# Optimization experiments

Measured on AMD Instinct MI355X. Metric: run time of the kernel, lower is better.

Reference implementation:

```python
import jax, jax.numpy as jnp
import numpy as np

D_MODEL = 1024
NUM_HEADS = 16
SEQ = 2048
BATCH = 4
THETA = 10000.0
D_K = D_MODEL // NUM_HEADS


def setup_inputs() -> dict:
    key = jax.random.key(0)
    k1, k2, k3, k4, k5 = jax.random.split(key, 5)
    std = np.sqrt(2.0 / (D_MODEL + D_MODEL))
    x = jax.random.normal(k1, (BATCH, SEQ, D_MODEL), dtype=jnp.float32)
    wq = jax.random.normal(k2, (D_MODEL, D_MODEL), dtype=jnp.float32) * std
    wk = jax.random.normal(k3, (D_MODEL, D_MODEL), dtype=jnp.float32) * std
    wv = jax.random.normal(k4, (D_MODEL, D_MODEL), dtype=jnp.float32) * std
    wo = jax.random.normal(k5, (D_MODEL, D_MODEL), dtype=jnp.float32) * std
    token_positions = jnp.arange(SEQ, dtype=jnp.int32)
    return {"x": x, "wq": wq, "wk": wk, "wv": wv, "wo": wo,
            "token_positions": token_positions}


def _apply_rope(t, cos, sin):
    # t: (b, h, s, d_k); cos/sin: (s, d_k/2) -> broadcast over (b, h)
    pairs = t.reshape(*t.shape[:-1], D_K // 2, 2)
    x0, x1 = pairs[..., 0], pairs[..., 1]
    r0 = x0 * cos - x1 * sin
    r1 = x0 * sin + x1 * cos
    return jnp.stack((r0, r1), axis=-1).reshape(t.shape)


def reference(x, wq, wk, wv, wo, token_positions):
    b, s, d = x.shape
    h, dk = NUM_HEADS, D_K

    def split_heads(y):  # (b, s, d) -> (b, h, s, d_k)
        return y.reshape(b, s, h, dk).transpose(0, 2, 1, 3)

    q = split_heads(x @ wq.T)
    k = split_heads(x @ wk.T)
    v = split_heads(x @ wv.T)

    # RoPE tables: angles_j = theta^{-(2j)/d_k}, j = 0..d_k/2-1
    inv_freq = 1.0 / (THETA ** (jnp.arange(0, dk, 2, dtype=jnp.float32) / dk))
    ang = token_positions.astype(jnp.float32)[:, None] * inv_freq[None, :]  # (s, d_k/2)
    cos, sin = jnp.cos(ang), jnp.sin(ang)
    q = _apply_rope(q, cos, sin)
    k = _apply_rope(k, cos, sin)

    scores = jnp.einsum('bhqd,bhkd->bhqk', q, k) / jnp.sqrt(jnp.float32(dk))
    causal = jnp.tril(jnp.ones((s, s), dtype=bool))
    scores = jnp.where(causal, scores, -jnp.inf)
    attn = jax.nn.softmax(scores, axis=-1)
    out = jnp.einsum('bhqk,bhkd->bhqd', attn, v)  # (b, h, s, d_k)
    out = out.transpose(0, 2, 1, 3).reshape(b, s, d)
    return out @ wo.T
```

## Files before the change

### kernel.cpp

```cpp
#include <hip/hip_runtime.h>
#include <stdint.h>

#define B_   4
#define S_   2048
#define H_   16
#define DK_  64
#define DM_  1024
#define M_   (B_ * S_)

typedef __attribute__((ext_vector_type(4)))  float f32x4;
typedef __attribute__((ext_vector_type(16))) float f32x16;
typedef __attribute__((ext_vector_type(8)))  short s16x8;

#define SCQ 0.18033688011112042f

__device__ __forceinline__ uint16_t f2bf(float f) {
    union { float f; uint32_t u; } v; v.f = f;
    uint32_t u = v.u;
    uint32_t r = (u + 0x7FFFu + ((u >> 16) & 1u)) >> 16;
    return (uint16_t)r;
}
__device__ __forceinline__ float bf2f(uint16_t h) {
    union { uint32_t u; float f; } v; v.u = ((uint32_t)h) << 16;
    return v.f;
}
__device__ __forceinline__ uint32_t cvt_pk_bf16(float lo, float hi) {
    uint32_t r;
    asm("v_cvt_pk_bf16_f32 %0, %1, %2" : "=v"(r) : "v"(lo), "v"(hi));
    return r;
}

__device__ __forceinline__ void gload_lds16(const uint16_t* g, uint16_t* l) {
    __builtin_amdgcn_global_load_lds(
        (const __attribute__((address_space(1))) void*)g,
        (__attribute__((address_space(3))) void*)l, 16, 0, 0);
}

__global__ __launch_bounds__(256) void cvt_all(const float* __restrict__ x,
                                               const float* __restrict__ w0,
                                               const float* __restrict__ w1,
                                               const float* __restrict__ w2,
                                               const float* __restrict__ w3,
                                               uint16_t* __restrict__ xo,
                                               uint16_t* __restrict__ o0,
                                               uint16_t* __restrict__ o1,
                                               uint16_t* __restrict__ o2,
                                               uint16_t* __restrict__ o3) {
    const size_t NX = (size_t)M_ * DM_;
    const size_t NW = (size_t)DM_ * DM_;
    size_t i = ((size_t)blockIdx.x * 256 + threadIdx.x) * 4;
    const float* in; uint16_t* out; size_t off;
    if (i < NX) { in = x; out = xo; off = i; }
    else {
        size_t j = i - NX;
        int sel = (int)(j >> 20);
        off = j & (NW - 1);
        in  = sel == 0 ? w0 : sel == 1 ? w1 : sel == 2 ? w2 : w3;
        out = sel == 0 ? o0 : sel == 1 ? o1 : sel == 2 ? o2 : o3;
    }
    float4 v = *reinterpret_cast<const float4*>(in + off);
    ushort4 o;
    o.x = f2bf(v.x); o.y = f2bf(v.y); o.z = f2bf(v.z); o.w = f2bf(v.w);
    *reinterpret_cast<ushort4*>(out + off) = o;
}

__global__ __launch_bounds__(256, 4) void gemm_qkv(const uint16_t* __restrict__ xb,
                                                   const uint16_t* __restrict__ wq,
                                                   const uint16_t* __restrict__ wk,
                                                   const uint16_t* __restrict__ wv,
                                                   uint16_t* __restrict__ qout,
                                                   uint16_t* __restrict__ kout,
                                                   uint16_t* __restrict__ vout) {
    __shared__ uint16_t Al[2][128 * 32];
    __shared__ uint16_t Bl[2][128 * 32];
    const int K = DM_;
    const int lane = threadIdx.x & 63;
    const int w    = threadIdx.x >> 6;
    const int wr   = w >> 1, wc = w & 1;
    const int sel  = blockIdx.x >> 3;
    const int np   = blockIdx.x & 7;
    const int y    = blockIdx.y;
    const int ql   = lane & 31;
    const int hi   = lane >> 5;

    const uint16_t* Aptr; const uint16_t* Bptr;
    int m0, n0;
    if (sel == 2) { Aptr = wv; Bptr = xb; m0 = np * 128; n0 = y * 128; }
    else          { Aptr = xb; Bptr = sel ? wk : wq; m0 = y * 128; n0 = np * 128; }

    const int srow = w * 32 + (lane >> 2);
    const int scol = (((lane & 3) ^ ((lane >> 3) & 3))) * 8;
    const uint16_t* Ag = Aptr + (size_t)(m0 + srow) * K + scol;
    const uint16_t* Bg = Bptr + (size_t)(n0 + srow) * K + scol;
    const int loff = w * 32 * 32;
    const int qsw  = (ql >> 1) & 3;

    f32x16 acc[2][2] = {};
#pragma unroll
    for (int i = 0; i < 2; ++i) {
        gload_lds16(Ag + (size_t)i * 16 * K, &Al[0][loff + i * 16 * 32]);
        gload_lds16(Bg + (size_t)i * 16 * K, &Bl[0][loff + i * 16 * 32]);
    }

    int cur = 0;
    for (int k0 = 0; k0 < K; k0 += 32) {
        __syncthreads();
        if (k0 + 32 < K) {
            const int nb = cur ^ 1, k2 = k0 + 32;
#pragma unroll
            for (int i = 0; i < 2; ++i) {
                gload_lds16(Ag + (size_t)i * 16 * K + k2, &Al[nb][loff + i * 16 * 32]);
                gload_lds16(Bg + (size_t)i * 16 * K + k2, &Bl[nb][loff + i * 16 * 32]);
            }
        }
        s16x8 af[2][2], bfr[2][2];
#pragma unroll
        for (int am = 0; am < 2; ++am)
#pragma unroll
            for (int ks = 0; ks < 2; ++ks)
                af[am][ks] = *reinterpret_cast<const s16x8*>(
                    &Al[cur][(wr * 64 + am * 32 + ql) * 32 + (((ks * 2 + hi) ^ qsw) * 8)]);
#pragma unroll
        for (int bn = 0; bn < 2; ++bn)
#pragma unroll
            for (int ks = 0; ks < 2; ++ks)
                bfr[bn][ks] = *reinterpret_cast<const s16x8*>(
                    &Bl[cur][(wc * 64 + bn * 32 + ql) * 32 + (((ks * 2 + hi) ^ qsw) * 8)]);
#pragma unroll
        for (int am = 0; am < 2; ++am)
#pragma unroll
            for (int bn = 0; bn < 2; ++bn) {
                acc[am][bn] = __builtin_amdgcn_mfma_f32_32x32x16_bf16(af[am][0], bfr[bn][0],
                                                                      acc[am][bn], 0, 0, 0);
                acc[am][bn] = __builtin_amdgcn_mfma_f32_32x32x16_bf16(af[am][1], bfr[bn][1],
                                                                      acc[am][bn], 0, 0, 0);
            }
        cur ^= 1;
    }

#pragma unroll
    for (int am = 0; am < 2; ++am)
#pragma unroll
        for (int bn = 0; bn < 2; ++bn)
#pragma unroll
            for (int r = 0; r < 16; ++r) {
                const int cr = (r & 3) + 8 * (r >> 2);
                int row = m0 + wr * 64 + am * 32 + 4 * hi + cr;
                int col = n0 + wc * 64 + bn * 32 + ql;
                float v = acc[am][bn][r];
                if (sel == 2) {
                    int h = row >> 6,  dk = row & 63;
                    int b = col >> 11, s = col & (S_ - 1);
                    vout[(((size_t)(b * H_ + h)) * DK_ + dk) * S_ + s] = f2bf(v);
                } else {
                    int b = row >> 11, s = row & (S_ - 1);
                    int h = col >> 6,  dk = col & 63;
                    uint16_t bv = f2bf(sel ? v : v * SCQ);
                    (sel ? kout : qout)[(((size_t)(b * H_ + h)) * S_ + s) * DK_ + dk] = bv;
                }
            }
}

__global__ __launch_bounds__(256, 4) void gemm_out(const uint16_t* __restrict__ A,
                                                   const uint16_t* __restrict__ Bm,
                                                   float* __restrict__ Cout,
                                                   int M, int N, int K) {
    __shared__ uint16_t Al[2][128 * 32];
    __shared__ uint16_t Bl[2][128 * 32];
    const int lane = threadIdx.x & 63;
    const int w    = threadIdx.x >> 6;
    const int wr   = w >> 1, wc = w & 1;
    const int m0   = blockIdx.x * 128;
    const int n0   = blockIdx.y * 128;
    const int ql   = lane & 31;
    const int hi   = lane >> 5;

    const int srow = w * 32 + (lane >> 2);
    const int scol = (((lane & 3) ^ ((lane >> 3) & 3))) * 8;
    const uint16_t* Ag = A  + (size_t)(m0 + srow) * K + scol;
    const uint16_t* Bg = Bm + (size_t)(n0 + srow) * K + scol;
    const int loff = w * 32 * 32;
    const int qsw  = (ql >> 1) & 3;

    f32x16 acc[2][2] = {};
#pragma unroll
    for (int i = 0; i < 2; ++i) {
        gload_lds16(Ag + (size_t)i * 16 * K, &Al[0][loff + i * 16 * 32]);
        gload_lds16(Bg + (size_t)i * 16 * K, &Bl[0][loff + i * 16 * 32]);
    }

    int cur = 0;
    for (int k0 = 0; k0 < K; k0 += 32) {
        __syncthreads();
        if (k0 + 32 < K) {
            const int nb = cur ^ 1, k2 = k0 + 32;
#pragma unroll
            for (int i = 0; i < 2; ++i) {
                gload_lds16(Ag + (size_t)i * 16 * K + k2, &Al[nb][loff + i * 16 * 32]);
                gload_lds16(Bg + (size_t)i * 16 * K + k2, &Bl[nb][loff + i * 16 * 32]);
            }
        }
        s16x8 af[2][2], bfr[2][2];
#pragma unroll
        for (int am = 0; am < 2; ++am)
#pragma unroll
            for (int ks = 0; ks < 2; ++ks)
                af[am][ks] = *reinterpret_cast<const s16x8*>(
                    &Al[cur][(wr * 64 + am * 32 + ql) * 32 + (((ks * 2 + hi) ^ qsw) * 8)]);
#pragma unroll
        for (int bn = 0; bn < 2; ++bn)
#pragma unroll
            for (int ks = 0; ks < 2; ++ks)
                bfr[bn][ks] = *reinterpret_cast<const s16x8*>(
                    &Bl[cur][(wc * 64 + bn * 32 + ql) * 32 + (((ks * 2 + hi) ^ qsw) * 8)]);
#pragma unroll
        for (int am = 0; am < 2; ++am)
#pragma unroll
            for (int bn = 0; bn < 2; ++bn) {
                acc[am][bn] = __builtin_amdgcn_mfma_f32_32x32x16_bf16(af[am][0], bfr[bn][0],
                                                                      acc[am][bn], 0, 0, 0);
                acc[am][bn] = __builtin_amdgcn_mfma_f32_32x32x16_bf16(af[am][1], bfr[bn][1],
                                                                      acc[am][bn], 0, 0, 0);
            }
        cur ^= 1;
    }

#pragma unroll
    for (int am = 0; am < 2; ++am)
#pragma unroll
        for (int bn = 0; bn < 2; ++bn)
#pragma unroll
            for (int r = 0; r < 16; ++r) {
                const int cr = (r & 3) + 8 * (r >> 2);
                int row = m0 + wr * 64 + am * 32 + 4 * hi + cr;
                int col = n0 + wc * 64 + bn * 32 + ql;
                Cout[(size_t)row * N + col] = acc[am][bn][r];
            }
}

__global__ __launch_bounds__(256) void rope_kernel(uint16_t* __restrict__ a,
                                                   const int* __restrict__ pos,
                                                   int npairs) {
    int t = blockIdx.x * 256 + threadIdx.x;
    if (t >= npairs) return;
    int j = t & 31;
    int s = (t >> 5) & (S_ - 1);
    float p   = (float)pos[s];
    float inv = exp2f(-(float)j * (13.287712379549449f / 32.0f));
    float ang = p * inv;
    float sn = __sinf(ang);
    float c  = __cosf(ang);
    uint32_t pr = *reinterpret_cast<uint32_t*>(a + (size_t)2 * t);
    float x0 = bf2f((uint16_t)(pr & 0xFFFF));
    float x1 = bf2f((uint16_t)(pr >> 16));
    float r0 = x0 * c - x1 * sn;
    float r1 = x0 * sn + x1 * c;
    uint32_t ot = (uint32_t)f2bf(r0) | ((uint32_t)f2bf(r1) << 16);
    *reinterpret_cast<uint32_t*>(a + (size_t)2 * t) = ot;
}

__global__ __launch_bounds__(256, 2) void flash_attn(const uint16_t* __restrict__ qg,
                                                     const uint16_t* __restrict__ kg,
                                                     const uint16_t* __restrict__ vtg,
                                                     const int* __restrict__ tpos,
                                                     uint16_t* __restrict__ attn) {
    __shared__ __align__(16) uint16_t Kl[2][4096];
    __shared__ __align__(16) uint16_t Vl[2][4096];
    const int lane = threadIdx.x & 63;
    const int w    = threadIdx.x >> 6;
    const int ql   = lane & 31;
    const int hi   = lane >> 5;
    const int id   = blockIdx.x;
    const int bh   = (id & 7) * 8 + ((id >> 3) & 7);
    const int s    = 15 - (id >> 6);
    const int b    = bh >> 4, hh = bh & 15;

    const uint16_t* kb_ = kg  + (size_t)bh * S_ * DK_;
    const uint16_t* vb_ = vtg + (size_t)bh * DK_ * S_;

    char* obb = (char*)&Kl[0][0] + w * 4096;
    const int swz = (ql & 7) << 4;

    const int q0 = s * 128 + w * 32;
    const int rowg  = q0 + ql;
    const int ntmax = 2 * s + 2;

    const int srow = lane >> 3;
    const int scol = ((lane & 7) ^ srow) << 3;

    const uint16_t* qp = qg + ((size_t)bh * S_ + q0 + ql) * DK_ + hi * 8;
    const float prow = (float)tpos[rowg];
    const float FR = 13.287712379549449f / 32.0f;
    s16x8 qf[4];
#pragma unroll
    for (int kk = 0; kk < 4; ++kk) {
        s16x8 raw = *reinterpret_cast<const s16x8*>(qp + kk * 16);
        union { uint32_t u[4]; s16x8 v; } pw;
#pragma unroll
        for (int jj = 0; jj < 4; ++jj) {
            float x0 = bf2f((uint16_t)raw[2 * jj]);
            float x1 = bf2f((uint16_t)raw[2 * jj + 1]);
            float ang = prow * exp2f(-(float)(kk * 8 + hi * 4 + jj) * FR);
            float sn = __sinf(ang), cs = __cosf(ang);
            pw.u[jj] = cvt_pk_bf16(x0 * cs - x1 * sn, x0 * sn + x1 * cs);
        }
        qf[kk] = pw.v;
    }

    f32x16 o0 = {}, o1 = {};
    float l_l = 0.f;

#pragma unroll
    for (int i = 0; i < 2; ++i) {
        gload_lds16(kb_ + (size_t)(w * 16 + i * 8 + srow) * DK_ + scol, &Kl[0][w * 1024 + i * 512]);
        gload_lds16(vb_ + (size_t)(w * 16 + i * 8 + srow) * S_  + scol, &Vl[0][w * 1024 + i * 512]);
    }

    for (int t = 0; t < ntmax; ++t) {
        const int kt  = t * 64;
        const int cur = t & 1;
        __syncthreads();
        if (t + 1 < ntmax) {
            const int kt2 = kt + 64, nb = cur ^ 1;
#pragma unroll
            for (int i = 0; i < 2; ++i) {
                gload_lds16(kb_ + (size_t)(kt2 + w * 16 + i * 8 + srow) * DK_ + scol,
                            &Kl[nb][w * 1024 + i * 512]);
                gload_lds16(vb_ + (size_t)(w * 16 + i * 8 + srow) * S_ + kt2 + scol,
                            &Vl[nb][w * 1024 + i * 512]);
            }
        }
        if (kt > q0 + 31) continue;

        s16x8 kf[8];
#pragma unroll
        for (int kb2 = 0; kb2 < 2; ++kb2)
#pragma unroll
            for (int kk = 0; kk < 4; ++kk)
                kf[kb2 * 4 + kk] = *reinterpret_cast<const s16x8*>(
                    &Kl[cur][(kb2 * 32 + ql) * 64 + (((kk * 32 + hi * 16) ^ swz) >> 1)]);

        f32x16 sc0 = {}, sc1 = {};
        __builtin_amdgcn_s_setprio(1);
#pragma unroll
        for (int kk = 0; kk < 4; ++kk)
            sc0 = __builtin_amdgcn_mfma_f32_32x32x16_bf16(kf[kk], qf[kk], sc0, 0, 0, 0);
#pragma unroll
        for (int kk = 0; kk < 4; ++kk)
            sc1 = __builtin_amdgcn_mfma_f32_32x32x16_bf16(kf[4 + kk], qf[kk], sc1, 0, 0, 0);
        __builtin_amdgcn_s_setprio(0);

        if (kt + 63 > q0) {
            const int keybase = kt + 4 * hi;
#pragma unroll
            for (int r = 0; r < 16; ++r) {
                const int cr = (r & 3) + 8 * (r >> 2);
                if (keybase + cr > rowg)      sc0[r] = -3e38f;
                if (keybase + cr + 32 > rowg) sc1[r] = -3e38f;
            }
        }

#pragma unroll
        for (int r = 0; r < 16; ++r) {
            float p0 = exp2f(sc0[r]);
            float p1 = exp2f(sc1[r]);
            sc0[r] = p0; sc1[r] = p1;
            l_l += p0 + p1;
        }

        s16x8 pf[4];
        {
            union PW { uint32_t u[4]; s16x8 v; };
#pragma unroll
            for (int half = 0; half < 2; ++half) {
                const f32x16& e = half ? sc1 : sc0;
#pragma unroll
                for (int sl = 0; sl < 2; ++sl) {
                    const int rb = sl * 8;
                    uint32_t a0 = cvt_pk_bf16(e[rb + 0], e[rb + 1]);
                    uint32_t b0 = cvt_pk_bf16(e[rb + 4], e[rb + 5]);
                    uint32_t a1 = cvt_pk_bf16(e[rb + 2], e[rb + 3]);
                    uint32_t b1 = cvt_pk_bf16(e[rb + 6], e[rb + 7]);
                    asm("v_permlane32_swap_b32 %0, %1" : "+v"(a0), "+v"(b0));
                    asm("v_permlane32_swap_b32 %0, %1" : "+v"(a1), "+v"(b1));
                    PW pw; pw.u[0] = a0; pw.u[1] = a1; pw.u[2] = b0; pw.u[3] = b1;
                    pf[half * 2 + sl] = pw.v;
                }
            }
        }

        s16x8 vf[8];
#pragma unroll
        for (int db = 0; db < 2; ++db)
#pragma unroll
            for (int ks = 0; ks < 4; ++ks)
                vf[db * 4 + ks] = *reinterpret_cast<const s16x8*>(
                    &Vl[cur][(db * 32 + ql) * 64 + (((ks * 32 + hi * 16) ^ swz) >> 1)]);

        __builtin_amdgcn_s_setprio(1);
#pragma unroll
        for (int ks = 0; ks < 4; ++ks) {
            o0 = __builtin_amdgcn_mfma_f32_32x32x16_bf16(vf[ks],     pf[ks], o0, 0, 0, 0);
            o1 = __builtin_amdgcn_mfma_f32_32x32x16_bf16(vf[4 + ks], pf[ks], o1, 0, 0, 0);
        }
        __builtin_amdgcn_s_setprio(0);
    }

    __syncthreads();

    l_l += __shfl_xor(l_l, 32);
    float rinv = 1.0f / l_l;

#pragma unroll
    for (int db = 0; db < 2; ++db) {
        const f32x16& o = db ? o1 : o0;
#pragma unroll
        for (int rq = 0; rq < 4; ++rq) {
            uint2 val;
            val.x = cvt_pk_bf16(o[4 * rq + 0] * rinv, o[4 * rq + 1] * rinv);
            val.y = cvt_pk_bf16(o[4 * rq + 2] * rinv, o[4 * rq + 3] * rinv);
            int colb = (db * 32 + 8 * rq + 4 * hi) * 2;
            *reinterpret_cast<uint2*>(obb + ql * 128 + (colb ^ swz)) = val;
        }
    }
    uint16_t* orow = attn + ((size_t)b * S_ + q0 + ql) * DM_ + hh * 64 + hi * 32;
#pragma unroll
    for (int i = 0; i < 4; ++i) {
        int colb = hi * 64 + i * 16;
        s16x8 vrow = *reinterpret_cast<const s16x8*>(obb + ql * 128 + (colb ^ swz));
        *reinterpret_cast<s16x8*>(orow + i * 8) = vrow;
    }
}

extern "C" void kernel_launch(void* const* d_in, const int* in_sizes, int n_in,
                              void* d_out, int out_size, void* d_ws, size_t ws_size,
                              hipStream_t stream) {
    (void)in_sizes; (void)n_in; (void)out_size;
    const float* x   = (const float*)d_in[0];
    const float* wq  = (const float*)d_in[1];
    const float* wk  = (const float*)d_in[2];
    const float* wv  = (const float*)d_in[3];
    const float* wo  = (const float*)d_in[4];
    const int* tpos  = (const int*)d_in[5];
    float* out = (float*)d_out;

    const size_t NX = (size_t)M_ * DM_;
    const size_t NW = (size_t)DM_ * DM_;
    const size_t need = (NX + 4 * NW + 4 * NX) * sizeof(uint16_t);
    if (ws_size < need) return;

    uint16_t* ws  = (uint16_t*)d_ws;
    uint16_t* xb  = ws;
    uint16_t* wqb = xb + NX;
    uint16_t* wkb = wqb + NW;
    uint16_t* wvb = wkb + NW;
    uint16_t* wob = wvb + NW;
    uint16_t* qb  = wob + NW;
    uint16_t* kb  = qb + NX;
    uint16_t* vtb = kb + NX;
    uint16_t* ab  = vtb + NX;

    cvt_all<<<(int)((NX + 4 * NW) / 1024), 256, 0, stream>>>(x, wq, wk, wv, wo,
                                                             xb, wqb, wkb, wvb, wob);

    gemm_qkv<<<dim3(24, M_ / 128), 256, 0, stream>>>(xb, wqb, wkb, wvb, qb, kb, vtb);

    int npairs_k = B_ * H_ * S_ * (DK_ / 2);
    rope_kernel<<<npairs_k / 256, 256, 0, stream>>>(kb, tpos, npairs_k);

    flash_attn<<<dim3(1024), 256, 0, stream>>>(qb, kb, vtb, tpos, ab);

    gemm_out<<<dim3(M_ / 128, DM_ / 128), 256, 0, stream>>>(ab, wob, out, M_, DM_, DM_);
}
```

Measured before the change: 192.5 us.

## Stage two K/V tiles per barrier in flash attention loop

The attention kernel now loads two 64-key K/V tiles per pipeline stage into double-buffered LDS and processes both before the next barrier. This halves the number of __syncthreads and prefetch issue points and gives each async load more compute to hide behind. LDS use doubles to 64KB per block, which may limit occupancy below the two blocks per CU requested by launch bounds.

```diff
diff --git a/kernel.cpp b/kernel.cpp
--- a/kernel.cpp
+++ b/kernel.cpp
@@ -264,8 +264,8 @@
                                                      const uint16_t* __restrict__ vtg,
                                                      const int* __restrict__ tpos,
                                                      uint16_t* __restrict__ attn) {
-    __shared__ __align__(16) uint16_t Kl[2][4096];
-    __shared__ __align__(16) uint16_t Vl[2][4096];
+    __shared__ __align__(16) uint16_t Kl[2][2][4096];
+    __shared__ __align__(16) uint16_t Vl[2][2][4096];
     const int lane = threadIdx.x & 63;
     const int w    = threadIdx.x >> 6;
     const int ql   = lane & 31;
@@ -278,7 +278,7 @@
     const uint16_t* kb_ = kg  + (size_t)bh * S_ * DK_;
     const uint16_t* vb_ = vtg + (size_t)bh * DK_ * S_;
 
-    char* obb = (char*)&Kl[0][0] + w * 4096;
+    char* obb = (char*)&Kl[0][0][0] + w * 4096;
     const int swz = (ql & 7) << 4;
 
     const int q0 = s * 128 + w * 32;
@@ -310,27 +310,8 @@
     f32x16 o0 = {}, o1 = {};
     float l_l = 0.f;
 
-#pragma unroll
-    for (int i = 0; i < 2; ++i) {
-        gload_lds16(kb_ + (size_t)(w * 16 + i * 8 + srow) * DK_ + scol, &Kl[0][w * 1024 + i * 512]);
-        gload_lds16(vb_ + (size_t)(w * 16 + i * 8 + srow) * S_  + scol, &Vl[0][w * 1024 + i * 512]);
-    }
-
-    for (int t = 0; t < ntmax; ++t) {
-        const int kt  = t * 64;
-        const int cur = t & 1;
-        __syncthreads();
-        if (t + 1 < ntmax) {
-            const int kt2 = kt + 64, nb = cur ^ 1;
-#pragma unroll
-            for (int i = 0; i < 2; ++i) {
-                gload_lds16(kb_ + (size_t)(kt2 + w * 16 + i * 8 + srow) * DK_ + scol,
-                            &Kl[nb][w * 1024 + i * 512]);
-                gload_lds16(vb_ + (size_t)(w * 16 + i * 8 + srow) * S_ + kt2 + scol,
-                            &Vl[nb][w * 1024 + i * 512]);
-            }
-        }
-        if (kt > q0 + 31) continue;
+    auto do_tile = [&](int kt, const uint16_t* Kh, const uint16_t* Vh) {
+        if (kt > q0 + 31) return;
 
         s16x8 kf[8];
 #pragma unroll
@@ -338,7 +319,7 @@
 #pragma unroll
             for (int kk = 0; kk < 4; ++kk)
                 kf[kb2 * 4 + kk] = *reinterpret_cast<const s16x8*>(
-                    &Kl[cur][(kb2 * 32 + ql) * 64 + (((kk * 32 + hi * 16) ^ swz) >> 1)]);
+                    &Kh[(kb2 * 32 + ql) * 64 + (((kk * 32 + hi * 16) ^ swz) >> 1)]);
 
         f32x16 sc0 = {}, sc1 = {};
         __builtin_amdgcn_s_setprio(1);
@@ -395,7 +376,7 @@
 #pragma unroll
             for (int ks = 0; ks < 4; ++ks)
                 vf[db * 4 + ks] = *reinterpret_cast<const s16x8*>(
-                    &Vl[cur][(db * 32 + ql) * 64 + (((ks * 32 + hi * 16) ^ swz) >> 1)]);
+                    &Vh[(db * 32 + ql) * 64 + (((ks * 32 + hi * 16) ^ swz) >> 1)]);
 
         __builtin_amdgcn_s_setprio(1);
 #pragma unroll
@@ -404,6 +385,39 @@
             o1 = __builtin_amdgcn_mfma_f32_32x32x16_bf16(vf[4 + ks], pf[ks], o1, 0, 0, 0);
         }
         __builtin_amdgcn_s_setprio(0);
+    };
+
+#pragma unroll
+    for (int half = 0; half < 2; ++half) {
+        const int kt2 = half * 64;
+#pragma unroll
+        for (int i = 0; i < 2; ++i) {
+            gload_lds16(kb_ + (size_t)(kt2 + w * 16 + i * 8 + srow) * DK_ + scol,
+                        &Kl[0][half][w * 1024 + i * 512]);
+            gload_lds16(vb_ + (size_t)(w * 16 + i * 8 + srow) * S_ + kt2 + scol,
+                        &Vl[0][half][w * 1024 + i * 512]);
+        }
+    }
+
+    for (int t = 0; t < ntmax; t += 2) {
+        const int cur = (t >> 1) & 1;
+        __syncthreads();
+        if (t + 2 < ntmax) {
+            const int nb = cur ^ 1;
+#pragma unroll
+            for (int half = 0; half < 2; ++half) {
+                const int kt2 = (t + 2 + half) * 64;
+#pragma unroll
+                for (int i = 0; i < 2; ++i) {
+                    gload_lds16(kb_ + (size_t)(kt2 + w * 16 + i * 8 + srow) * DK_ + scol,
+                                &Kl[nb][half][w * 1024 + i * 512]);
+                    gload_lds16(vb_ + (size_t)(w * 16 + i * 8 + srow) * S_ + kt2 + scol,
+                                &Vl[nb][half][w * 1024 + i * 512]);
+                }
+            }
+        }
+        do_tile(t * 64,       &Kl[cur][0][0], &Vl[cur][0][0]);
+        do_tile((t + 1) * 64, &Kl[cur][1][0], &Vl[cur][1][0]);
     }
 
     __syncthreads();
```

New measurement: 193.6 us. No clear change (+0.5%).
